# Kernel tuning notes

Hardware: AMD Instinct MI355X
Metric: run time of the kernel (lower is better)

## Reference

```python
import jax, jax.numpy as jnp
import numpy as np

B, S, T, C = 4, 2048, 2048, 256
TEMPERATURE = 0.1
CONF_THR = 0.2
NEG_INF = -jnp.inf


def setup_inputs() -> dict:
    key = jax.random.key(0)
    k1, k2, k3 = jax.random.split(key, 3)
    src_feats = jax.random.normal(k1, (B, S, C), dtype=jnp.float32)
    tgt_feats = jax.random.normal(k2, (B, T, C), dtype=jnp.float32)
    # variable valid lengths per batch (padding masks)
    src_lens = jnp.array([2048, 1800, 1500, 1024])
    tgt_lens = jnp.array([2048, 1600, 2000, 1200])
    src_mask = jnp.arange(S)[None, :] < src_lens[:, None]
    tgt_mask = jnp.arange(T)[None, :] < tgt_lens[:, None]
    W = jax.random.normal(k3, (C, C), dtype=jnp.float32) * (C ** -0.5)
    return {"src_feats": src_feats, "tgt_feats": tgt_feats,
            "src_mask": src_mask, "tgt_mask": tgt_mask, "W": W}


def reference(src_feats, tgt_feats, src_mask, tgt_mask, W):
    # NOTE: original module applies src_proj to BOTH src and tgt (tgt_proj unused)
    src = jnp.einsum('bsc,dc->bsd', src_feats, W)  # Linear, no bias
    tgt = jnp.einsum('btc,dc->btd', tgt_feats, W)
    scale = src.shape[-1] ** 0.5
    src = src / scale
    tgt = tgt / scale
    sim = jnp.einsum('bsc,btc->bst', src, tgt) / TEMPERATURE  # [B,S,T]
    sim1 = jnp.where(src_mask[:, :, None], sim, NEG_INF)
    sim2 = jnp.where(tgt_mask[:, None, :], sim, NEG_INF)
    conf_matrix = jax.nn.softmax(sim1, axis=1) * jax.nn.softmax(sim2, axis=2)
    # get_match (no_grad in original): mutual-max + threshold mask.
    # Returned as a dense boolean mask (jit-safe), instead of nonzero() indices.
    m = conf_matrix > CONF_THR
    m = m & (conf_matrix == jnp.max(conf_matrix, axis=2, keepdims=True)) \
          & (conf_matrix == jnp.max(conf_matrix, axis=1, keepdims=True))
    return conf_matrix, m
```

## Files before the change

### kernel.cpp

```cpp
#include <hip/hip_runtime.h>
#include <hip/hip_bf16.h>
#include <cstdint>
#include <cstddef>

#define B_ 4
#define S_ 2048
#define T_ 2048
#define C_ 256
#define NEG_INF (-INFINITY)

typedef __attribute__((ext_vector_type(8)))  __bf16 bf16x8;
typedef __attribute__((ext_vector_type(4)))  __bf16 bf16x4;
typedef __attribute__((ext_vector_type(16))) float  f32x16;

#define ROWPAT(r, lh) (((r) & 3) + 8 * ((r) >> 2) + 4 * (lh))

__global__ void build_masks_kernel(const void* __restrict__ src_mask,
                                   const void* __restrict__ tgt_mask,
                                   int* __restrict__ smask, int* __restrict__ tmask) {
    int i = blockIdx.x * blockDim.x + threadIdx.x;
    const unsigned char* sb = (const unsigned char*)src_mask;
    const unsigned char* tb = (const unsigned char*)tgt_mask;
    bool s_is_byte = (sb[1] != 0);
    bool t_is_byte = (tb[1] != 0);
    if (i < B_ * S_)
        smask[i] = s_is_byte ? (sb[i] != 0) : (((const int*)src_mask)[i] != 0);
    if (i < B_ * T_)
        tmask[i] = t_is_byte ? (tb[i] != 0) : (((const int*)tgt_mask)[i] != 0);
}

__global__ __launch_bounds__(256) void split_kernel(
    const float* __restrict__ in, __bf16* __restrict__ h, __bf16* __restrict__ l,
    int n4)
{
    for (int i = blockIdx.x * blockDim.x + threadIdx.x; i < n4;
         i += gridDim.x * blockDim.x) {
        float4 x = ((const float4*)in)[i];
        float xs[4] = {x.x, x.y, x.z, x.w};
        bf16x4 hv, lv;
        #pragma unroll
        for (int j = 0; j < 4; ++j) {
            __bf16 hh = (__bf16)xs[j];
            hv[j] = hh;
            lv[j] = (__bf16)(xs[j] - (float)hh);
        }
        ((bf16x4*)h)[i] = hv;
        ((bf16x4*)l)[i] = lv;
    }
}

#define MFMA3(i, j)                                                              \
    acc[i][j] = __builtin_amdgcn_mfma_f32_32x32x16_bf16(ah[i], bh[j], acc[i][j], 0, 0, 0); \
    acc[i][j] = __builtin_amdgcn_mfma_f32_32x32x16_bf16(ah[i], bl[j], acc[i][j], 0, 0, 0); \
    acc[i][j] = __builtin_amdgcn_mfma_f32_32x32x16_bf16(al[i], bh[j], acc[i][j], 0, 0, 0);

__global__ __launch_bounds__(256) void proj_kernel(
    const __bf16* __restrict__ Fh, const __bf16* __restrict__ Fl,
    const __bf16* __restrict__ Wh, const __bf16* __restrict__ Wl,
    __bf16* __restrict__ Ph, __bf16* __restrict__ Pl)
{
    const int n0 = blockIdx.x * 128, m0 = blockIdx.y * 128;
    const int w = threadIdx.x >> 6, lane = threadIdx.x & 63;
    const int wr = w >> 1, wc = w & 1;
    const int lr = lane & 31, lh = lane >> 5;

    const size_t aoff0 = (size_t)(m0 + 64 * wr + lr) * C_ + 8 * lh;
    const size_t aoff1 = aoff0 + 32 * C_;
    const size_t boff0 = (size_t)(n0 + 64 * wc + lr) * C_ + 8 * lh;
    const size_t boff1 = boff0 + 32 * C_;

    f32x16 acc[2][2] = {};
    #pragma unroll 2
    for (int ks = 0; ks < 16; ++ks) {
        const int kk = ks * 16;
        bf16x8 ah[2], al[2], bh[2], bl[2];
        ah[0] = *(const bf16x8*)(Fh + aoff0 + kk);
        ah[1] = *(const bf16x8*)(Fh + aoff1 + kk);
        al[0] = *(const bf16x8*)(Fl + aoff0 + kk);
        al[1] = *(const bf16x8*)(Fl + aoff1 + kk);
        bh[0] = *(const bf16x8*)(Wh + boff0 + kk);
        bh[1] = *(const bf16x8*)(Wh + boff1 + kk);
        bl[0] = *(const bf16x8*)(Wl + boff0 + kk);
        bl[1] = *(const bf16x8*)(Wl + boff1 + kk);
        MFMA3(0, 0) MFMA3(0, 1) MFMA3(1, 0) MFMA3(1, 1)
    }

    #pragma unroll
    for (int i = 0; i < 2; ++i)
        #pragma unroll
        for (int j = 0; j < 2; ++j)
            #pragma unroll
            for (int r = 0; r < 16; ++r) {
                float v = acc[i][j][r] * 0.0625f;
                __bf16 hh = (__bf16)v;
                int row = m0 + 64 * wr + 32 * i + ROWPAT(r, lh);
                int col = n0 + 64 * wc + 32 * j + lr;
                Ph[(size_t)row * C_ + col] = hh;
                Pl[(size_t)row * C_ + col] = (__bf16)(v - (float)hh);
            }
}

template <int MODE>
__global__ __launch_bounds__(256) void simgemm_kernel(
    const __bf16* __restrict__ Ah_, const __bf16* __restrict__ Al_,
    const __bf16* __restrict__ Bh_, const __bf16* __restrict__ Bl_,
    const int* __restrict__ smask, const int* __restrict__ tmask,
    float2* __restrict__ rowpart, float2* __restrict__ colpart,
    const float2* __restrict__ rowstats, const float2* __restrict__ colstats,
    float* __restrict__ conf, unsigned* __restrict__ rowconfmax,
    unsigned* __restrict__ colconfmax)
{
    const int b = blockIdx.z;
    const int n0 = blockIdx.x * 128, m0 = blockIdx.y * 128;
    const int w = threadIdx.x >> 6, lane = threadIdx.x & 63;
    const int wr = w >> 1, wc = w & 1;
    const int lr = lane & 31, lh = lane >> 5;

    __shared__ int smask_lds[128], tmask_lds[128];
    __shared__ float2 rstat_lds[128], cstat_lds[128];
    if (threadIdx.x < 128) {
        smask_lds[threadIdx.x] = smask[b * S_ + m0 + threadIdx.x];
        if (MODE == 1) rstat_lds[threadIdx.x] = rowstats[b * S_ + m0 + threadIdx.x];
    } else {
        int t = threadIdx.x - 128;
        tmask_lds[t] = tmask[b * T_ + n0 + t];
        if (MODE == 1) cstat_lds[t] = colstats[b * T_ + n0 + t];
    }
    __syncthreads();

    const __bf16* Ah = Ah_ + (size_t)b * S_ * C_;
    const __bf16* Al = Al_ + (size_t)b * S_ * C_;
    const __bf16* Bh = Bh_ + (size_t)b * T_ * C_;
    const __bf16* Bl = Bl_ + (size_t)b * T_ * C_;

    const size_t aoff0 = (size_t)(m0 + 64 * wr + lr) * C_ + 8 * lh;
    const size_t aoff1 = aoff0 + 32 * C_;
    const size_t boff0 = (size_t)(n0 + 64 * wc + lr) * C_ + 8 * lh;
    const size_t boff1 = boff0 + 32 * C_;

    f32x16 acc[2][2] = {};
    #pragma unroll 2
    for (int ks = 0; ks < 16; ++ks) {
        const int kk = ks * 16;
        bf16x8 ah[2], al[2], bh[2], bl[2];
        ah[0] = *(const bf16x8*)(Ah + aoff0 + kk);
        ah[1] = *(const bf16x8*)(Ah + aoff1 + kk);
        al[0] = *(const bf16x8*)(Al + aoff0 + kk);
        al[1] = *(const bf16x8*)(Al + aoff1 + kk);
        bh[0] = *(const bf16x8*)(Bh + boff0 + kk);
        bh[1] = *(const bf16x8*)(Bh + boff1 + kk);
        bl[0] = *(const bf16x8*)(Bl + boff0 + kk);
        bl[1] = *(const bf16x8*)(Bl + boff1 + kk);
        MFMA3(0, 0) MFMA3(0, 1) MFMA3(1, 0) MFMA3(1, 1)
    }

    if (MODE == 0) {
        const int tm0 = tmask_lds[64 * wc + lr];
        const int tm1 = tmask_lds[64 * wc + 32 + lr];
        #pragma unroll
        for (int i = 0; i < 2; ++i) {
            #pragma unroll
            for (int r = 0; r < 16; ++r) {
                float v0 = tm0 ? acc[i][0][r] * 10.f : NEG_INF;
                float v1 = tm1 ? acc[i][1][r] * 10.f : NEG_INF;
                float m = fmaxf(v0, v1);
                #pragma unroll
                for (int off = 1; off <= 16; off <<= 1)
                    m = fmaxf(m, __shfl_xor(m, off));
                float e = 0.f;
                if (m > NEG_INF) e = __expf(v0 - m) + __expf(v1 - m);
                #pragma unroll
                for (int off = 1; off <= 16; off <<= 1)
                    e += __shfl_xor(e, off);
                if (lr == 0) {
                    int row = m0 + 64 * wr + 32 * i + ROWPAT(r, lh);
                    rowpart[((size_t)(b * S_ + row)) * 32 + (n0 >> 6) + wc] =
                        make_float2(m, e);
                }
            }
        }
        #pragma unroll
        for (int j = 0; j < 2; ++j) {
            float m = NEG_INF;
            #pragma unroll
            for (int i = 0; i < 2; ++i)
                #pragma unroll
                for (int r = 0; r < 16; ++r) {
                    int sm = smask_lds[64 * wr + 32 * i + ROWPAT(r, lh)];
                    float x = sm ? acc[i][j][r] * 10.f : NEG_INF;
                    m = fmaxf(m, x);
                }
            m = fmaxf(m, __shfl_xor(m, 32));
            float e = 0.f;
            if (m > NEG_INF) {
                #pragma unroll
                for (int i = 0; i < 2; ++i)
                    #pragma unroll
                    for (int r = 0; r < 16; ++r) {
                        int sm = smask_lds[64 * wr + 32 * i + ROWPAT(r, lh)];
                        float x = sm ? acc[i][j][r] * 10.f : NEG_INF;
                        e += __expf(x - m);
                    }
            }
            e += __shfl_xor(e, 32);
            if (lh == 0) {
                int col = n0 + 64 * wc + 32 * j + lr;
                colpart[((size_t)(b * T_ + col)) * 32 + (m0 >> 6) + wr] =
                    make_float2(m, e);
            }
        }
    } else {
        const int tm0 = tmask_lds[64 * wc + lr];
        const int tm1 = tmask_lds[64 * wc + 32 + lr];
        float2 cst0 = cstat_lds[64 * wc + lr];
        float2 cst1 = cstat_lds[64 * wc + 32 + lr];
        const float cm0 = cst0.x, invc0 = 1.f / cst0.y;
        const float cm1 = cst1.x, invc1 = 1.f / cst1.y;
        float* confb = conf + (size_t)b * S_ * T_;
        float cmax0 = 0.f, cmax1 = 0.f;
        #pragma unroll
        for (int i = 0; i < 2; ++i) {
            #pragma unroll
            for (int r = 0; r < 16; ++r) {
                int row_l = 64 * wr + 32 * i + ROWPAT(r, lh);
                float2 rst = rstat_lds[row_l];
                int sm = smask_lds[row_l];
                float rm = rst.x, invr = 1.f / rst.y;
                float v0 = acc[i][0][r] * 10.f;
                float v1 = acc[i][1][r] * 10.f;
                float c0 = (sm && tm0)
                    ? __expf(2.f * v0 - cm0 - rm) * (invc0 * invr) : 0.f;
                float c1 = (sm && tm1)
                    ? __expf(2.f * v1 - cm1 - rm) * (invc1 * invr) : 0.f;
                int row_g = m0 + row_l;
                int col0 = n0 + 64 * wc + lr;
                confb[(size_t)row_g * T_ + col0]      = c0;
                confb[(size_t)row_g * T_ + col0 + 32] = c1;
                float rmx = fmaxf(c0, c1);
                #pragma unroll
                for (int off = 1; off <= 16; off <<= 1)
                    rmx = fmaxf(rmx, __shfl_xor(rmx, off));
                if (lr == 0)
                    atomicMax(&rowconfmax[b * S_ + row_g], __float_as_uint(rmx));
                cmax0 = fmaxf(cmax0, c0);
                cmax1 = fmaxf(cmax1, c1);
            }
        }
        cmax0 = fmaxf(cmax0, __shfl_xor(cmax0, 32));
        cmax1 = fmaxf(cmax1, __shfl_xor(cmax1, 32));
        if (lh == 0) {
            int col0 = n0 + 64 * wc + lr;
            atomicMax(&colconfmax[b * T_ + col0],      __float_as_uint(cmax0));
            atomicMax(&colconfmax[b * T_ + col0 + 32], __float_as_uint(cmax1));
        }
    }
}

__global__ __launch_bounds__(256) void combine_kernel(
    const float2* __restrict__ part, float2* __restrict__ stats, int nrow)
{
    int r = blockIdx.x * 256 + threadIdx.x;
    if (r >= nrow) return;
    const float2* p = part + (size_t)r * 32;
    float M = NEG_INF;
    float2 v[32];
    #pragma unroll
    for (int q = 0; q < 16; ++q) {
        float4 f = *(const float4*)(p + q * 2);
        v[2 * q]     = make_float2(f.x, f.y);
        v[2 * q + 1] = make_float2(f.z, f.w);
    }
    #pragma unroll
    for (int q = 0; q < 32; ++q) M = fmaxf(M, v[q].x);
    float SS = 0.f;
    if (M > NEG_INF) {
        #pragma unroll
        for (int q = 0; q < 32; ++q) SS += v[q].y * __expf(v[q].x - M);
    }
    stats[r] = make_float2(M, SS);
}

__global__ __launch_bounds__(256) void maskout_kernel(
    const float* __restrict__ conf,
    const unsigned* __restrict__ rowconfmax, const unsigned* __restrict__ colconfmax,
    float* __restrict__ outmask)
{
    const size_t n4 = (size_t)B_ * S_ * T_ / 4;
    for (size_t i4 = (size_t)blockIdx.x * blockDim.x + threadIdx.x; i4 < n4;
         i4 += (size_t)gridDim.x * blockDim.x) {
        size_t base = i4 * 4;
        int t0  = (int)(base & (T_ - 1));
        int row = (int)(base >> 11);
        int b   = row >> 11;
        float4 c = *(const float4*)(conf + base);
        float rm = __uint_as_float(rowconfmax[row]);
        const unsigned* cmp = colconfmax + b * T_ + t0;
        float cc[4] = {c.x, c.y, c.z, c.w};
        float o[4];
        #pragma unroll
        for (int j = 0; j < 4; ++j) {
            float cmv = __uint_as_float(cmp[j]);
            o[j] = (cc[j] > 0.2f && cc[j] == rm && cc[j] == cmv) ? 1.f : 0.f;
        }
        *(float4*)(outmask + base) = make_float4(o[0], o[1], o[2], o[3]);
    }
}

extern "C" void kernel_launch(void* const* d_in, const int* in_sizes, int n_in,
                              void* d_out, int out_size, void* d_ws, size_t ws_size,
                              hipStream_t stream)
{
    const float* src_feats = (const float*)d_in[0];
    const float* tgt_feats = (const float*)d_in[1];
    const void*  src_mask  = d_in[2];
    const void*  tgt_mask  = d_in[3];
    const float* W         = (const float*)d_in[4];

    float* conf    = (float*)d_out;
    char*  maskreg = (char*)d_out + (size_t)B_ * S_ * T_ * 4;

    const size_t MB = 1024 * 1024;
    __bf16* srcf_h = (__bf16*)(maskreg + 0 * MB);
    __bf16* srcf_l = (__bf16*)(maskreg + 4 * MB);
    __bf16* tgtf_h = (__bf16*)(maskreg + 8 * MB);
    __bf16* tgtf_l = (__bf16*)(maskreg + 12 * MB);
    __bf16* srcp_h = (__bf16*)(maskreg + 16 * MB);
    __bf16* srcp_l = (__bf16*)(maskreg + 20 * MB);
    __bf16* tgtp_h = (__bf16*)(maskreg + 24 * MB);
    __bf16* tgtp_l = (__bf16*)(maskreg + 28 * MB);
    __bf16* W_h    = (__bf16*)(maskreg + 32 * MB);
    __bf16* W_l    = (__bf16*)(maskreg + 32 * MB + 128 * 1024);
    float2* rowpart = (float2*)(maskreg + 33 * MB);
    float2* colpart = (float2*)(maskreg + 35 * MB);

    float2*   rowstats   = (float2*)d_ws;
    float2*   colstats   = rowstats + B_ * S_;
    unsigned* rowconfmax = (unsigned*)(colstats + B_ * T_);
    unsigned* colconfmax = rowconfmax + B_ * S_;
    int*      smask      = (int*)(colconfmax + B_ * T_);
    int*      tmask      = smask + B_ * S_;

    hipMemsetAsync(rowconfmax, 0, (size_t)(B_ * S_ + B_ * T_) * sizeof(unsigned),
                   stream);
    build_masks_kernel<<<(B_ * S_ + 255) / 256, 256, 0, stream>>>(
        src_mask, tgt_mask, smask, tmask);

    split_kernel<<<1024, 256, 0, stream>>>(src_feats, srcf_h, srcf_l,
                                           B_ * S_ * C_ / 4);
    split_kernel<<<1024, 256, 0, stream>>>(tgt_feats, tgtf_h, tgtf_l,
                                           B_ * T_ * C_ / 4);
    split_kernel<<<64, 256, 0, stream>>>(W, W_h, W_l, C_ * C_ / 4);

    proj_kernel<<<dim3(C_ / 128, B_ * S_ / 128), 256, 0, stream>>>(
        srcf_h, srcf_l, W_h, W_l, srcp_h, srcp_l);
    proj_kernel<<<dim3(C_ / 128, B_ * T_ / 128), 256, 0, stream>>>(
        tgtf_h, tgtf_l, W_h, W_l, tgtp_h, tgtp_l);

    simgemm_kernel<0><<<dim3(T_ / 128, S_ / 128, B_), 256, 0, stream>>>(
        srcp_h, srcp_l, tgtp_h, tgtp_l, smask, tmask, rowpart, colpart,
        nullptr, nullptr, nullptr, nullptr, nullptr);

    combine_kernel<<<(B_ * S_ + 255) / 256, 256, 0, stream>>>(
        rowpart, rowstats, B_ * S_);
    combine_kernel<<<(B_ * T_ + 255) / 256, 256, 0, stream>>>(
        colpart, colstats, B_ * T_);

    simgemm_kernel<1><<<dim3(T_ / 128, S_ / 128, B_), 256, 0, stream>>>(
        srcp_h, srcp_l, tgtp_h, tgtp_l, smask, tmask, nullptr, nullptr,
        rowstats, colstats, conf, rowconfmax, colconfmax);

    maskout_kernel<<<4096, 256, 0, stream>>>(conf, rowconfmax, colconfmax,
                                             (float*)maskreg);
}
```

Measured before the change: 376.5 us.

## Interleave bf16 hi/lo split and stage GEMM tiles through LDS with async loads

Stores the hi/lo bf16 split interleaved as pairs, so one K=512 operand carries both parts. The three-MFMA product is computed as two passes: A against B, and A against B with each hi/lo pair swapped. The similarity GEMMs move to 256x256 tiles with 512 threads, double-buffered through XOR-swizzled LDS using global_load_lds, and a remapped block order. The projection reuses the same kernel (mode 2), replacing the separate proj_kernel. The aim is to cut global-memory operand reloads and raise MFMA reuse, at the cost of a larger LDS footprint and an extra lo*lo term in the product.

```diff
diff --git a/kernel.cpp b/kernel.cpp
--- a/kernel.cpp
+++ b/kernel.cpp
@@ -7,13 +7,28 @@
 #define S_ 2048
 #define T_ 2048
 #define C_ 256
+#define K2_ 512
 #define NEG_INF (-INFINITY)
 
 typedef __attribute__((ext_vector_type(8)))  __bf16 bf16x8;
-typedef __attribute__((ext_vector_type(4)))  __bf16 bf16x4;
 typedef __attribute__((ext_vector_type(16))) float  f32x16;
 
 #define ROWPAT(r, lh) (((r) & 3) + 8 * ((r) >> 2) + 4 * (lh))
+
+typedef __attribute__((address_space(3))) unsigned       as3_u32;
+typedef __attribute__((address_space(1))) const unsigned as1_u32;
+
+__device__ __forceinline__ void gload16(const void* g, void* l) {
+    __builtin_amdgcn_global_load_lds((as1_u32*)g, (as3_u32*)l, 16, 0, 0);
+}
+
+__device__ __forceinline__ unsigned pack_hl(float v) {
+    __bf16 h = (__bf16)v;
+    __bf16 l = (__bf16)(v - (float)h);
+    unsigned short hu = __builtin_bit_cast(unsigned short, h);
+    unsigned short lu = __builtin_bit_cast(unsigned short, l);
+    return (unsigned)hu | ((unsigned)lu << 16);
+}
 
 __global__ void build_masks_kernel(const void* __restrict__ src_mask,
                                    const void* __restrict__ tgt_mask,
@@ -30,139 +45,145 @@
 }
 
 __global__ __launch_bounds__(256) void split_kernel(
-    const float* __restrict__ in, __bf16* __restrict__ h, __bf16* __restrict__ l,
-    int n4)
+    const float* __restrict__ in, unsigned* __restrict__ out, int n4)
 {
     for (int i = blockIdx.x * blockDim.x + threadIdx.x; i < n4;
          i += gridDim.x * blockDim.x) {
         float4 x = ((const float4*)in)[i];
-        float xs[4] = {x.x, x.y, x.z, x.w};
-        bf16x4 hv, lv;
-        #pragma unroll
-        for (int j = 0; j < 4; ++j) {
-            __bf16 hh = (__bf16)xs[j];
-            hv[j] = hh;
-            lv[j] = (__bf16)(xs[j] - (float)hh);
-        }
-        ((bf16x4*)h)[i] = hv;
-        ((bf16x4*)l)[i] = lv;
-    }
-}
-
-#define MFMA3(i, j)                                                              \
-    acc[i][j] = __builtin_amdgcn_mfma_f32_32x32x16_bf16(ah[i], bh[j], acc[i][j], 0, 0, 0); \
-    acc[i][j] = __builtin_amdgcn_mfma_f32_32x32x16_bf16(ah[i], bl[j], acc[i][j], 0, 0, 0); \
-    acc[i][j] = __builtin_amdgcn_mfma_f32_32x32x16_bf16(al[i], bh[j], acc[i][j], 0, 0, 0);
-
-__global__ __launch_bounds__(256) void proj_kernel(
-    const __bf16* __restrict__ Fh, const __bf16* __restrict__ Fl,
-    const __bf16* __restrict__ Wh, const __bf16* __restrict__ Wl,
-    __bf16* __restrict__ Ph, __bf16* __restrict__ Pl)
-{
-    const int n0 = blockIdx.x * 128, m0 = blockIdx.y * 128;
-    const int w = threadIdx.x >> 6, lane = threadIdx.x & 63;
-    const int wr = w >> 1, wc = w & 1;
-    const int lr = lane & 31, lh = lane >> 5;
-
-    const size_t aoff0 = (size_t)(m0 + 64 * wr + lr) * C_ + 8 * lh;
-    const size_t aoff1 = aoff0 + 32 * C_;
-    const size_t boff0 = (size_t)(n0 + 64 * wc + lr) * C_ + 8 * lh;
-    const size_t boff1 = boff0 + 32 * C_;
-
-    f32x16 acc[2][2] = {};
-    #pragma unroll 2
-    for (int ks = 0; ks < 16; ++ks) {
-        const int kk = ks * 16;
-        bf16x8 ah[2], al[2], bh[2], bl[2];
-        ah[0] = *(const bf16x8*)(Fh + aoff0 + kk);
-        ah[1] = *(const bf16x8*)(Fh + aoff1 + kk);
-        al[0] = *(const bf16x8*)(Fl + aoff0 + kk);
-        al[1] = *(const bf16x8*)(Fl + aoff1 + kk);
-        bh[0] = *(const bf16x8*)(Wh + boff0 + kk);
-        bh[1] = *(const bf16x8*)(Wh + boff1 + kk);
-        bl[0] = *(const bf16x8*)(Wl + boff0 + kk);
-        bl[1] = *(const bf16x8*)(Wl + boff1 + kk);
-        MFMA3(0, 0) MFMA3(0, 1) MFMA3(1, 0) MFMA3(1, 1)
-    }
-
-    #pragma unroll
-    for (int i = 0; i < 2; ++i)
-        #pragma unroll
-        for (int j = 0; j < 2; ++j)
-            #pragma unroll
-            for (int r = 0; r < 16; ++r) {
-                float v = acc[i][j][r] * 0.0625f;
-                __bf16 hh = (__bf16)v;
-                int row = m0 + 64 * wr + 32 * i + ROWPAT(r, lh);
-                int col = n0 + 64 * wc + 32 * j + lr;
-                Ph[(size_t)row * C_ + col] = hh;
-                Pl[(size_t)row * C_ + col] = (__bf16)(v - (float)hh);
-            }
+        uint4 o;
+        o.x = pack_hl(x.x); o.y = pack_hl(x.y);
+        o.z = pack_hl(x.z); o.w = pack_hl(x.w);
+        ((uint4*)out)[i] = o;
+    }
 }
 
 template <int MODE>
-__global__ __launch_bounds__(256) void simgemm_kernel(
-    const __bf16* __restrict__ Ah_, const __bf16* __restrict__ Al_,
-    const __bf16* __restrict__ Bh_, const __bf16* __restrict__ Bl_,
+__global__ __launch_bounds__(512, 2) void simgemm_kernel(
+    const __bf16* __restrict__ A2g, const __bf16* __restrict__ B2g,
     const int* __restrict__ smask, const int* __restrict__ tmask,
     float2* __restrict__ rowpart, float2* __restrict__ colpart,
     const float2* __restrict__ rowstats, const float2* __restrict__ colstats,
     float* __restrict__ conf, unsigned* __restrict__ rowconfmax,
-    unsigned* __restrict__ colconfmax)
-{
-    const int b = blockIdx.z;
-    const int n0 = blockIdx.x * 128, m0 = blockIdx.y * 128;
-    const int w = threadIdx.x >> 6, lane = threadIdx.x & 63;
-    const int wr = w >> 1, wc = w & 1;
+    unsigned* __restrict__ colconfmax, unsigned* __restrict__ P2out)
+{
+    __shared__ char lds[2 * 65536 + 256 * 4 * 2 + 256 * 8 * 2];
+    char* bufs = lds;
+    int*    smask_lds = (int*)(lds + 131072);
+    int*    tmask_lds = smask_lds + 256;
+    float2* rstat_lds = (float2*)(tmask_lds + 256);
+    float2* cstat_lds = rstat_lds + 256;
+
+    const int tid = threadIdx.x;
+    const int w = tid >> 6, lane = tid & 63;
+    const int wr = w >> 2, wc = w & 3;
     const int lr = lane & 31, lh = lane >> 5;
 
-    __shared__ int smask_lds[128], tmask_lds[128];
-    __shared__ float2 rstat_lds[128], cstat_lds[128];
-    if (threadIdx.x < 128) {
-        smask_lds[threadIdx.x] = smask[b * S_ + m0 + threadIdx.x];
-        if (MODE == 1) rstat_lds[threadIdx.x] = rowstats[b * S_ + m0 + threadIdx.x];
+    int b = 0, m0, n0;
+    const __bf16 *Ab, *Bb;
+    if (MODE == 2) {
+        m0 = blockIdx.x * 256; n0 = 0;
+        Ab = A2g; Bb = B2g;
     } else {
-        int t = threadIdx.x - 128;
-        tmask_lds[t] = tmask[b * T_ + n0 + t];
-        if (MODE == 1) cstat_lds[t] = colstats[b * T_ + n0 + t];
-    }
+        int lin = (blockIdx.x & 7) * 32 + (blockIdx.x >> 3);
+        b = lin >> 6;
+        int r = lin & 63;
+        m0 = (r >> 3) * 256;
+        n0 = (r & 7) * 256;
+        Ab = A2g + (size_t)b * S_ * K2_;
+        Bb = B2g + (size_t)b * T_ * K2_;
+        if (tid < 256) {
+            smask_lds[tid] = smask[b * S_ + m0 + tid];
+            if (MODE == 1) rstat_lds[tid] = rowstats[b * S_ + m0 + tid];
+        } else {
+            int t = tid - 256;
+            tmask_lds[t] = tmask[b * T_ + n0 + t];
+            if (MODE == 1) cstat_lds[t] = colstats[b * T_ + n0 + t];
+        }
+    }
+
+    auto stage = [&](int st) {
+        char* buf = bufs + (st & 1) * 65536;
+        const int kb = st * 64;
+        #pragma unroll
+        for (int q = 0; q < 4; ++q) {
+            int i = q * 512 + tid;
+            int row = i >> 3, c = i & 7;
+            int sc = c ^ (row & 7);
+            gload16(Ab + (size_t)(m0 + row) * K2_ + kb + sc * 8,
+                    buf + (q * 512 + w * 64) * 16);
+        }
+        char* bufB = buf + 32768;
+        #pragma unroll
+        for (int q = 0; q < 4; ++q) {
+            int i = q * 512 + tid;
+            int row = i >> 3, c = i & 7;
+            int sc = c ^ (row & 7);
+            gload16(Bb + (size_t)(n0 + row) * K2_ + kb + sc * 8,
+                    bufB + (q * 512 + w * 64) * 16);
+        }
+    };
+
+    f32x16 acc[4][2] = {};
+    stage(0);
     __syncthreads();
-
-    const __bf16* Ah = Ah_ + (size_t)b * S_ * C_;
-    const __bf16* Al = Al_ + (size_t)b * S_ * C_;
-    const __bf16* Bh = Bh_ + (size_t)b * T_ * C_;
-    const __bf16* Bl = Bl_ + (size_t)b * T_ * C_;
-
-    const size_t aoff0 = (size_t)(m0 + 64 * wr + lr) * C_ + 8 * lh;
-    const size_t aoff1 = aoff0 + 32 * C_;
-    const size_t boff0 = (size_t)(n0 + 64 * wc + lr) * C_ + 8 * lh;
-    const size_t boff1 = boff0 + 32 * C_;
-
-    f32x16 acc[2][2] = {};
-    #pragma unroll 2
-    for (int ks = 0; ks < 16; ++ks) {
-        const int kk = ks * 16;
-        bf16x8 ah[2], al[2], bh[2], bl[2];
-        ah[0] = *(const bf16x8*)(Ah + aoff0 + kk);
-        ah[1] = *(const bf16x8*)(Ah + aoff1 + kk);
-        al[0] = *(const bf16x8*)(Al + aoff0 + kk);
-        al[1] = *(const bf16x8*)(Al + aoff1 + kk);
-        bh[0] = *(const bf16x8*)(Bh + boff0 + kk);
-        bh[1] = *(const bf16x8*)(Bh + boff1 + kk);
-        bl[0] = *(const bf16x8*)(Bl + boff0 + kk);
-        bl[1] = *(const bf16x8*)(Bl + boff1 + kk);
-        MFMA3(0, 0) MFMA3(0, 1) MFMA3(1, 0) MFMA3(1, 1)
+    for (int st = 0; st < 8; ++st) {
+        if (st < 7) stage(st + 1);
+        const char* buf  = bufs + (st & 1) * 65536;
+        const char* bufB = buf + 32768;
+        #pragma unroll
+        for (int ks = 0; ks < 4; ++ks) {
+            const int cs = ks * 2 + lh;
+            bf16x8 a[4], bv[2], bs[2];
+            #pragma unroll
+            for (int fi = 0; fi < 4; ++fi) {
+                int row = wr * 128 + fi * 32 + lr;
+                a[fi] = *(const bf16x8*)(buf + row * 128 + ((cs ^ (row & 7)) * 16));
+            }
+            #pragma unroll
+            for (int fj = 0; fj < 2; ++fj) {
+                int row = wc * 64 + fj * 32 + lr;
+                bv[fj] = *(const bf16x8*)(bufB + row * 128 + ((cs ^ (row & 7)) * 16));
+                bs[fj] = __builtin_shufflevector(bv[fj], bv[fj], 1, 0, 3, 2, 5, 4, 7, 6);
+            }
+            #pragma unroll
+            for (int fi = 0; fi < 4; ++fi)
+                #pragma unroll
+                for (int fj = 0; fj < 2; ++fj)
+                    acc[fi][fj] = __builtin_amdgcn_mfma_f32_32x32x16_bf16(
+                        a[fi], bv[fj], acc[fi][fj], 0, 0, 0);
+            #pragma unroll
+            for (int fi = 0; fi < 4; ++fi)
+                #pragma unroll
+                for (int fj = 0; fj < 2; ++fj)
+                    acc[fi][fj] = __builtin_amdgcn_mfma_f32_32x32x16_bf16(
+                        a[fi], bs[fj], acc[fi][fj], 0, 0, 0);
+        }
+        __syncthreads();
+    }
+
+    if (MODE == 2) {
+        #pragma unroll
+        for (int fi = 0; fi < 4; ++fi)
+            #pragma unroll
+            for (int fj = 0; fj < 2; ++fj)
+                #pragma unroll
+                for (int r = 0; r < 16; ++r) {
+                    int row = m0 + wr * 128 + fi * 32 + ROWPAT(r, lh);
+                    int col = wc * 64 + fj * 32 + lr;
+                    P2out[(size_t)row * 256 + col] = pack_hl(acc[fi][fj][r] * 0.0625f);
+                }
+        return;
     }
 
     if (MODE == 0) {
-        const int tm0 = tmask_lds[64 * wc + lr];
-        const int tm1 = tmask_lds[64 * wc + 32 + lr];
-        #pragma unroll
-        for (int i = 0; i < 2; ++i) {
+        const int tm0 = tmask_lds[wc * 64 + lr];
+        const int tm1 = tmask_lds[wc * 64 + 32 + lr];
+        #pragma unroll
+        for (int fi = 0; fi < 4; ++fi)
             #pragma unroll
             for (int r = 0; r < 16; ++r) {
-                float v0 = tm0 ? acc[i][0][r] * 10.f : NEG_INF;
-                float v1 = tm1 ? acc[i][1][r] * 10.f : NEG_INF;
+                float v0 = tm0 ? acc[fi][0][r] * 10.f : NEG_INF;
+                float v1 = tm1 ? acc[fi][1][r] * 10.f : NEG_INF;
                 float m = fmaxf(v0, v1);
                 #pragma unroll
                 for (int off = 1; off <= 16; off <<= 1)
@@ -173,110 +194,101 @@
                 for (int off = 1; off <= 16; off <<= 1)
                     e += __shfl_xor(e, off);
                 if (lr == 0) {
-                    int row = m0 + 64 * wr + 32 * i + ROWPAT(r, lh);
+                    int row = m0 + wr * 128 + fi * 32 + ROWPAT(r, lh);
                     rowpart[((size_t)(b * S_ + row)) * 32 + (n0 >> 6) + wc] =
                         make_float2(m, e);
                 }
             }
-        }
-        #pragma unroll
-        for (int j = 0; j < 2; ++j) {
+        #pragma unroll
+        for (int fj = 0; fj < 2; ++fj) {
             float m = NEG_INF;
             #pragma unroll
-            for (int i = 0; i < 2; ++i)
+            for (int fi = 0; fi < 4; ++fi)
                 #pragma unroll
                 for (int r = 0; r < 16; ++r) {
-                    int sm = smask_lds[64 * wr + 32 * i + ROWPAT(r, lh)];
-                    float x = sm ? acc[i][j][r] * 10.f : NEG_INF;
+                    int rl = wr * 128 + fi * 32 + ROWPAT(r, lh);
+                    float x = smask_lds[rl] ? acc[fi][fj][r] * 10.f : NEG_INF;
                     m = fmaxf(m, x);
                 }
             m = fmaxf(m, __shfl_xor(m, 32));
             float e = 0.f;
             if (m > NEG_INF) {
                 #pragma unroll
-                for (int i = 0; i < 2; ++i)
+                for (int fi = 0; fi < 4; ++fi)
                     #pragma unroll
                     for (int r = 0; r < 16; ++r) {
-                        int sm = smask_lds[64 * wr + 32 * i + ROWPAT(r, lh)];
-                        float x = sm ? acc[i][j][r] * 10.f : NEG_INF;
+                        int rl = wr * 128 + fi * 32 + ROWPAT(r, lh);
+                        float x = smask_lds[rl] ? acc[fi][fj][r] * 10.f : NEG_INF;
                         e += __expf(x - m);
                     }
             }
             e += __shfl_xor(e, 32);
             if (lh == 0) {
-                int col = n0 + 64 * wc + 32 * j + lr;
-                colpart[((size_t)(b * T_ + col)) * 32 + (m0 >> 6) + wr] =
+                int col = n0 + wc * 64 + fj * 32 + lr;
+                colpart[((size_t)(b * T_ + col)) * 16 + (m0 >> 7) + wr] =
                     make_float2(m, e);
             }
         }
-    } else {
-        const int tm0 = tmask_lds[64 * wc + lr];
-        const int tm1 = tmask_lds[64 * wc + 32 + lr];
-        float2 cst0 = cstat_lds[64 * wc + lr];
-        float2 cst1 = cstat_lds[64 * wc + 32 + lr];
-        const float cm0 = cst0.x, invc0 = 1.f / cst0.y;
-        const float cm1 = cst1.x, invc1 = 1.f / cst1.y;
+        return;
+    }
+
+    {
+        const int tm0 = tmask_lds[wc * 64 + lr];
+        const int tm1 = tmask_lds[wc * 64 + 32 + lr];
+        float2 c0 = cstat_lds[wc * 64 + lr];
+        float2 c1 = cstat_lds[wc * 64 + 32 + lr];
+        const float cm0 = c0.x, ic0 = 1.f / c0.y;
+        const float cm1 = c1.x, ic1 = 1.f / c1.y;
         float* confb = conf + (size_t)b * S_ * T_;
         float cmax0 = 0.f, cmax1 = 0.f;
         #pragma unroll
-        for (int i = 0; i < 2; ++i) {
+        for (int fi = 0; fi < 4; ++fi)
             #pragma unroll
             for (int r = 0; r < 16; ++r) {
-                int row_l = 64 * wr + 32 * i + ROWPAT(r, lh);
-                float2 rst = rstat_lds[row_l];
-                int sm = smask_lds[row_l];
-                float rm = rst.x, invr = 1.f / rst.y;
-                float v0 = acc[i][0][r] * 10.f;
-                float v1 = acc[i][1][r] * 10.f;
-                float c0 = (sm && tm0)
-                    ? __expf(2.f * v0 - cm0 - rm) * (invc0 * invr) : 0.f;
-                float c1 = (sm && tm1)
-                    ? __expf(2.f * v1 - cm1 - rm) * (invc1 * invr) : 0.f;
-                int row_g = m0 + row_l;
-                int col0 = n0 + 64 * wc + lr;
-                confb[(size_t)row_g * T_ + col0]      = c0;
-                confb[(size_t)row_g * T_ + col0 + 32] = c1;
-                float rmx = fmaxf(c0, c1);
+                int rl = wr * 128 + fi * 32 + ROWPAT(r, lh);
+                float2 rst = rstat_lds[rl];
+                int sm = smask_lds[rl];
+                float rm = rst.x, ir = 1.f / rst.y;
+                float x0 = acc[fi][0][r] * 10.f;
+                float x1 = acc[fi][1][r] * 10.f;
+                float cv0 = (sm && tm0)
+                    ? __expf(2.f * x0 - cm0 - rm) * (ic0 * ir) : 0.f;
+                float cv1 = (sm && tm1)
+                    ? __expf(2.f * x1 - cm1 - rm) * (ic1 * ir) : 0.f;
+                int rg = m0 + rl;
+                int cg = n0 + wc * 64 + lr;
+                confb[(size_t)rg * T_ + cg]      = cv0;
+                confb[(size_t)rg * T_ + cg + 32] = cv1;
+                float rmx = fmaxf(cv0, cv1);
                 #pragma unroll
                 for (int off = 1; off <= 16; off <<= 1)
                     rmx = fmaxf(rmx, __shfl_xor(rmx, off));
                 if (lr == 0)
-                    atomicMax(&rowconfmax[b * S_ + row_g], __float_as_uint(rmx));
-                cmax0 = fmaxf(cmax0, c0);
-                cmax1 = fmaxf(cmax1, c1);
-            }
-        }
+                    atomicMax(&rowconfmax[b * S_ + rg], __float_as_uint(rmx));
+                cmax0 = fmaxf(cmax0, cv0);
+                cmax1 = fmaxf(cmax1, cv1);
+            }
         cmax0 = fmaxf(cmax0, __shfl_xor(cmax0, 32));
         cmax1 = fmaxf(cmax1, __shfl_xor(cmax1, 32));
         if (lh == 0) {
-            int col0 = n0 + 64 * wc + lr;
-            atomicMax(&colconfmax[b * T_ + col0],      __float_as_uint(cmax0));
-            atomicMax(&colconfmax[b * T_ + col0 + 32], __float_as_uint(cmax1));
+            int cg = n0 + wc * 64 + lr;
+            atomicMax(&colconfmax[b * T_ + cg],      __float_as_uint(cmax0));
+            atomicMax(&colconfmax[b * T_ + cg + 32], __float_as_uint(cmax1));
         }
     }
 }
 
 __global__ __launch_bounds__(256) void combine_kernel(
-    const float2* __restrict__ part, float2* __restrict__ stats, int nrow)
+    const float2* __restrict__ part, float2* __restrict__ stats, int n, int width)
 {
     int r = blockIdx.x * 256 + threadIdx.x;
-    if (r >= nrow) return;
-    const float2* p = part + (size_t)r * 32;
+    if (r >= n) return;
+    const float2* p = part + (size_t)r * width;
     float M = NEG_INF;
-    float2 v[32];
-    #pragma unroll
-    for (int q = 0; q < 16; ++q) {
-        float4 f = *(const float4*)(p + q * 2);
-        v[2 * q]     = make_float2(f.x, f.y);
-        v[2 * q + 1] = make_float2(f.z, f.w);
-    }
-    #pragma unroll
-    for (int q = 0; q < 32; ++q) M = fmaxf(M, v[q].x);
+    for (int q = 0; q < width; ++q) M = fmaxf(M, p[q].x);
     float SS = 0.f;
-    if (M > NEG_INF) {
-        #pragma unroll
-        for (int q = 0; q < 32; ++q) SS += v[q].y * __expf(v[q].x - M);
-    }
+    if (M > NEG_INF)
+        for (int q = 0; q < width; ++q) SS += p[q].y * __expf(p[q].x - M);
     stats[r] = make_float2(M, SS);
 }
 
@@ -320,18 +332,16 @@
     char*  maskreg = (char*)d_out + (size_t)B_ * S_ * T_ * 4;
 
     const size_t MB = 1024 * 1024;
-    __bf16* srcf_h = (__bf16*)(maskreg + 0 * MB);
-    __bf16* srcf_l = (__bf16*)(maskreg + 4 * MB);
-    __bf16* tgtf_h = (__bf16*)(maskreg + 8 * MB);
-    __bf16* tgtf_l = (__bf16*)(maskreg + 12 * MB);
-    __bf16* srcp_h = (__bf16*)(maskreg + 16 * MB);
-    __bf16* srcp_l = (__bf16*)(maskreg + 20 * MB);
-    __bf16* tgtp_h = (__bf16*)(maskreg + 24 * MB);
-    __bf16* tgtp_l = (__bf16*)(maskreg + 28 * MB);
-    __bf16* W_h    = (__bf16*)(maskreg + 32 * MB);
-    __bf16* W_l    = (__bf16*)(maskreg + 32 * MB + 128 * 1024);
-    float2* rowpart = (float2*)(maskreg + 33 * MB);
-    float2* colpart = (float2*)(maskreg + 35 * MB);
+    unsigned* feats2u = (unsigned*)(maskreg);
+    unsigned* P2u     = (unsigned*)(maskreg + 16 * MB);
+    unsigned* W2u     = (unsigned*)(maskreg + 32 * MB);
+    float2* rowpart   = (float2*)(maskreg + 33 * MB);
+    float2* colpart   = (float2*)(maskreg + 35 * MB);
+
+    const __bf16* feats2 = (const __bf16*)feats2u;
+    const __bf16* W2     = (const __bf16*)W2u;
+    const __bf16* P2src  = (const __bf16*)P2u;
+    const __bf16* P2tgt  = P2src + (size_t)B_ * S_ * K2_;
 
     float2*   rowstats   = (float2*)d_ws;
     float2*   colstats   = rowstats + B_ * S_;
@@ -345,30 +355,28 @@
     build_masks_kernel<<<(B_ * S_ + 255) / 256, 256, 0, stream>>>(
         src_mask, tgt_mask, smask, tmask);
 
-    split_kernel<<<1024, 256, 0, stream>>>(src_feats, srcf_h, srcf_l,
-                                           B_ * S_ * C_ / 4);
-    split_kernel<<<1024, 256, 0, stream>>>(tgt_feats, tgtf_h, tgtf_l,
-                                           B_ * T_ * C_ / 4);
-    split_kernel<<<64, 256, 0, stream>>>(W, W_h, W_l, C_ * C_ / 4);
-
-    proj_kernel<<<dim3(C_ / 128, B_ * S_ / 128), 256, 0, stream>>>(
-        srcf_h, srcf_l, W_h, W_l, srcp_h, srcp_l);
-    proj_kernel<<<dim3(C_ / 128, B_ * T_ / 128), 256, 0, stream>>>(
-        tgtf_h, tgtf_l, W_h, W_l, tgtp_h, tgtp_l);
-
-    simgemm_kernel<0><<<dim3(T_ / 128, S_ / 128, B_), 256, 0, stream>>>(
-        srcp_h, srcp_l, tgtp_h, tgtp_l, smask, tmask, rowpart, colpart,
-        nullptr, nullptr, nullptr, nullptr, nullptr);
+    split_kernel<<<2048, 256, 0, stream>>>(src_feats, feats2u, B_ * S_ * C_ / 4);
+    split_kernel<<<2048, 256, 0, stream>>>(
+        tgt_feats, feats2u + (size_t)B_ * S_ * C_, B_ * T_ * C_ / 4);
+    split_kernel<<<64, 256, 0, stream>>>(W, W2u, C_ * C_ / 4);
+
+    simgemm_kernel<2><<<(2 * B_ * S_) / 256, 512, 0, stream>>>(
+        feats2, W2, nullptr, nullptr, nullptr, nullptr, nullptr, nullptr,
+        nullptr, nullptr, nullptr, P2u);
+
+    simgemm_kernel<0><<<(S_ / 256) * (T_ / 256) * B_, 512, 0, stream>>>(
+        P2src, P2tgt, smask, tmask, rowpart, colpart,
+        nullptr, nullptr, nullptr, nullptr, nullptr, nullptr);
 
     combine_kernel<<<(B_ * S_ + 255) / 256, 256, 0, stream>>>(
-        rowpart, rowstats, B_ * S_);
+        rowpart, rowstats, B_ * S_, 32);
     combine_kernel<<<(B_ * T_ + 255) / 256, 256, 0, stream>>>(
-        colpart, colstats, B_ * T_);
-
-    simgemm_kernel<1><<<dim3(T_ / 128, S_ / 128, B_), 256, 0, stream>>>(
-        srcp_h, srcp_l, tgtp_h, tgtp_l, smask, tmask, nullptr, nullptr,
-        rowstats, colstats, conf, rowconfmax, colconfmax);
-
-    maskout_kernel<<<4096, 256, 0, stream>>>(conf, rowconfmax, colconfmax,
+        colpart, colstats, B_ * T_, 16);
+
+    simgemm_kernel<1><<<(S_ / 256) * (T_ / 256) * B_, 512, 0, stream>>>(
+        P2src, P2tgt, smask, tmask, nullptr, nullptr,
+        rowstats, colstats, conf, rowconfmax, colconfmax, nullptr);
+
+    maskout_kernel<<<2048, 256, 0, stream>>>(conf, rowconfmax, colconfmax,
                                              (float*)maskreg);
 }
```

Result: faster. 304.0 us (-19.2%).
